# Optimization experiments

Measured on AMD Instinct MI355X. Metric: run time of the kernel, lower is better.

Reference implementation:

```python
import jax, jax.numpy as jnp
import numpy as np

N = 100000
E = 1600000
IN_F, HID_F, OUT_F = 64, 64, 32
NEG_SLOPE = 0.01  # torch F.leaky_relu default


def setup_inputs() -> dict:
    key = jax.random.key(0)
    ks = jax.random.split(key, 8)
    feats = jax.random.normal(ks[0], (N, IN_F), dtype=jnp.float32)
    edge_src = jax.random.randint(ks[1], (E,), 0, N, dtype=jnp.int32)
    edge_dst = jax.random.randint(ks[2], (E,), 0, N, dtype=jnp.int32)
    edge_weight = jax.random.uniform(ks[3], (E,), dtype=jnp.float32)
    # Linear params (torch nn.Linear init scale ~ 1/sqrt(fan_in))
    W1 = jax.random.normal(ks[4], (IN_F, HID_F), dtype=jnp.float32) / np.sqrt(IN_F)
    b1 = jnp.zeros((HID_F,), dtype=jnp.float32)
    W2 = jax.random.normal(ks[5], (HID_F, OUT_F), dtype=jnp.float32) / np.sqrt(HID_F)
    b2 = jnp.zeros((OUT_F,), dtype=jnp.float32)
    return {
        "feats": feats,
        "edge_src": edge_src,
        "edge_dst": edge_dst,
        "edge_weight": edge_weight,
        "W1": W1,
        "b1": b1,
        "W2": W2,
        "b2": b2,
    }


def _aggregate(x, edge_src, edge_dst, edge_weight):
    # (A @ x) with A given as a weighted edge list: out[dst] += w * x[src]
    msgs = x[edge_src] * edge_weight[:, None]          # [E, F]
    return jax.ops.segment_sum(msgs, edge_dst, num_segments=N)  # [N, F]


def reference(feats, edge_src, edge_dst, edge_weight, W1, b1, W2, b2):
    h = _aggregate(feats, edge_src, edge_dst, edge_weight) @ W1 + b1  # conv1(A @ feats)
    h = jnp.where(h >= 0, h, NEG_SLOPE * h)                            # leaky_relu
    h = _aggregate(h, edge_src, edge_dst, edge_weight) @ W2 + b2       # conv2(A @ h)
    return h
```

## Files before the change

### kernel.cpp

```cpp
#include <hip/hip_runtime.h>
#include <hip/hip_fp16.h>

#define NN 100000
#define NE 1600000
#define NEG_SLOPE 0.01f

#define NTL(x) __builtin_nontemporal_load(&(x))
typedef float fvec4 __attribute__((ext_vector_type(4)));
typedef float fvec2 __attribute__((ext_vector_type(2)));
typedef short bf16x8 __attribute__((ext_vector_type(8)));
typedef float f32x4 __attribute__((ext_vector_type(4)));

#define NB     391
#define TILE   4096
#define NTILES 391
#define CAP    8192

#define G1_BLOCKS 512
#define G1_WAVES  (G1_BLOCKS * 4)
#define G1_TILES  6250

#define OFF_BCNT  400384
#define OFF_BOFFS 402432
#define OFF_GCUR  404432
#define OFF_CSR   408384
#define OFF_YQ    6808384
#define OFF_HW    19608384

__global__ __launch_bounds__(256) void k_bucketcnt(const int* __restrict__ dst,
                                                   int* __restrict__ bcnt)
{
    __shared__ int h[NB];
    int t = threadIdx.x;
    for (int i = t; i < NB; i += 256) h[i] = 0;
    __syncthreads();
    int base = blockIdx.x * TILE;
    for (int i = t; i < TILE; i += 256) {
        int e = base + i;
        if (e < NE) atomicAdd(&h[NTL(dst[e]) >> 8], 1);
    }
    __syncthreads();
    for (int i = t; i < NB; i += 256)
        if (h[i]) atomicAdd(&bcnt[i], h[i]);
}

__global__ __launch_bounds__(512) void k_bucketscan(const int* __restrict__ bcnt,
                                                    int* __restrict__ boffs,
                                                    int* __restrict__ gcur)
{
    __shared__ int lds[512];
    int t = threadIdx.x;
    int v = (t < NB) ? bcnt[t] : 0;
    lds[t] = v;
    __syncthreads();
    for (int off = 1; off < 512; off <<= 1) {
        int x = (t >= off) ? lds[t - off] : 0;
        __syncthreads();
        lds[t] += x;
        __syncthreads();
    }
    int excl = lds[t] - v;
    if (t < NB) { boffs[t] = excl; gcur[t] = excl; }
    if (t == NB - 1) boffs[NB] = lds[t];
}

__global__ __launch_bounds__(256) void k_binscatter(const int* __restrict__ dst,
                                                    const int* __restrict__ esrc,
                                                    const float* __restrict__ ew,
                                                    int* __restrict__ gcur,
                                                    int2* __restrict__ binned)
{
    __shared__ int   hist[NB];
    __shared__ int   cstart[NB];
    __shared__ int   ccur[NB];
    __shared__ int   gb[NB];
    __shared__ int   lds2[256];
    __shared__ int   sdst[TILE];
    __shared__ short sbuck[TILE];
    __shared__ int2  stage[TILE];

    int t = threadIdx.x;
    int base = blockIdx.x * TILE;
    int nvalid = NE - base; if (nvalid > TILE) nvalid = TILE;

    for (int i = t; i < NB; i += 256) hist[i] = 0;
    __syncthreads();
    for (int i = t; i < TILE; i += 256) {
        int e = base + i;
        int d = (e < NE) ? NTL(dst[e]) : -1;
        sdst[i] = d;
        if (d >= 0) atomicAdd(&hist[d >> 8], 1);
    }
    __syncthreads();

    int h0 = (2 * t     < NB) ? hist[2 * t]     : 0;
    int h1 = (2 * t + 1 < NB) ? hist[2 * t + 1] : 0;
    int ps = h0 + h1;
    lds2[t] = ps;
    __syncthreads();
    for (int off = 1; off < 256; off <<= 1) {
        int x = (t >= off) ? lds2[t - off] : 0;
        __syncthreads();
        lds2[t] += x;
        __syncthreads();
    }
    int excl = lds2[t] - ps;
    if (2 * t     < NB) { cstart[2 * t]     = excl;      ccur[2 * t]     = excl; }
    if (2 * t + 1 < NB) { cstart[2 * t + 1] = excl + h0; ccur[2 * t + 1] = excl + h0; }
    __syncthreads();

    for (int i = t; i < TILE; i += 256) {
        int d = sdst[i];
        if (d >= 0) {
            int e = base + i;
            int b = d >> 8;
            int pos = atomicAdd(&ccur[b], 1);
            stage[pos] = make_int2((NTL(esrc[e]) << 8) | (d & 255),
                                   __float_as_int(NTL(ew[e])));
            sbuck[pos] = (short)b;
        }
    }
    __syncthreads();

    for (int i = t; i < NB; i += 256)
        if (hist[i]) gb[i] = atomicAdd(&gcur[i], hist[i]);
    __syncthreads();
    for (int i = t; i < nvalid; i += 256) {
        int b = sbuck[i];
        binned[gb[b] + (i - cstart[b])] = stage[i];
    }
}

__global__ __launch_bounds__(256) void k_bucketsort(const int2* __restrict__ binned,
                                                    const int* __restrict__ boffs,
                                                    int* __restrict__ offs,
                                                    int* __restrict__ csrp)
{
    __shared__ int nhist[256];
    __shared__ int nstart[256];
    __shared__ int ncur[256];
    __shared__ int lds[256];
    __shared__ int stage[CAP];

    int t = threadIdx.x, b = blockIdx.x;
    int s0 = boffs[b], s1 = boffs[b + 1];
    int cnt = s1 - s0;

    nhist[t] = 0;
    __syncthreads();
    for (int i = t; i < cnt; i += 256)
        atomicAdd(&nhist[binned[s0 + i].x & 255], 1);
    __syncthreads();

    int v = nhist[t];
    lds[t] = v;
    __syncthreads();
    for (int off = 1; off < 256; off <<= 1) {
        int x = (t >= off) ? lds[t - off] : 0;
        __syncthreads();
        lds[t] += x;
        __syncthreads();
    }
    int excl = lds[t] - v;
    nstart[t] = excl;
    ncur[t] = excl;
    int node = b * 256 + t;
    if (node < NN) offs[node] = s0 + excl;
    if (b == NB - 1 && t == 0) offs[NN] = s1;
    __syncthreads();

    for (int i = t; i < cnt; i += 256) {
        int2 r = binned[s0 + i];
        int dl = r.x & 255;
        unsigned src = ((unsigned)r.x) >> 8;
        float w = __int_as_float(r.y);
        unsigned wq = (unsigned)(w * 32767.0f + 0.5f);
        int pos = atomicAdd(&ncur[dl], 1);
        stage[pos] = (int)((src << 15) | wq);
    }
    __syncthreads();
    for (int i = t; i < cnt; i += 256)
        csrp[s0 + i] = stage[i];
}

__device__ __forceinline__ short f2bf(float x)
{
    unsigned u = __float_as_uint(x);
    u += 0x7FFFu + ((u >> 16) & 1u);
    return (short)(u >> 16);
}

__global__ __launch_bounds__(256) void k_gemm1(const float* __restrict__ feats,
                                               const float* __restrict__ W1,
                                               unsigned char* __restrict__ Yq)
{
    int lane = threadIdx.x & 63;
    int wid = (blockIdx.x * 256 + threadIdx.x) >> 6;
    int rc = lane & 15;
    int kg = lane >> 4;

    bf16x8 bfr[4][2];
    #pragma unroll
    for (int nt = 0; nt < 4; ++nt)
        #pragma unroll
        for (int kc = 0; kc < 2; ++kc) {
            int k0 = kc * 32 + kg * 8;
            #pragma unroll
            for (int b = 0; b < 8; ++b)
                bfr[nt][kc][b] = f2bf(W1[(k0 + b) * 64 + nt * 16 + rc]);
        }

    for (int t = wid; t < G1_TILES; t += G1_WAVES) {
        const float* ar = feats + (t * 16 + rc) * 64;
        bf16x8 af[2];
        #pragma unroll
        for (int kc = 0; kc < 2; ++kc) {
            const float4 v0 = *(const float4*)(ar + kc * 32 + kg * 8);
            const float4 v1 = *(const float4*)(ar + kc * 32 + kg * 8 + 4);
            af[kc][0] = f2bf(v0.x); af[kc][1] = f2bf(v0.y);
            af[kc][2] = f2bf(v0.z); af[kc][3] = f2bf(v0.w);
            af[kc][4] = f2bf(v1.x); af[kc][5] = f2bf(v1.y);
            af[kc][6] = f2bf(v1.z); af[kc][7] = f2bf(v1.w);
        }
        #pragma unroll
        for (int nt = 0; nt < 4; ++nt) {
            f32x4 acc = {0.f, 0.f, 0.f, 0.f};
            acc = __builtin_amdgcn_mfma_f32_16x16x32_bf16(af[0], bfr[nt][0], acc, 0, 0, 0);
            acc = __builtin_amdgcn_mfma_f32_16x16x32_bf16(af[1], bfr[nt][1], acc, 0, 0, 0);
            #pragma unroll
            for (int r = 0; r < 4; ++r) {
                int orow = t * 16 + kg * 4 + r;
                int b8 = __builtin_amdgcn_cvt_pk_fp8_f32(acc[r], acc[r], 0, false) & 0xFF;
                Yq[orow * 64 + nt * 16 + rc] = (unsigned char)b8;
            }
        }
    }
}

#define WDEC(c) ((float)((c) & 0x7fffu) * (1.0f / 32767.0f))

__global__ __launch_bounds__(256) void k_l1(const int* __restrict__ offs,
                                            const int* __restrict__ csrp,
                                            const unsigned char* __restrict__ Yq,
                                            const float* __restrict__ b1,
                                            const float* __restrict__ W2,
                                            __half* __restrict__ hw)
{
    __shared__ __align__(16) float sh[4][4][64];
    int tid = threadIdx.x;
    int lane = tid & 63;
    int wv = tid >> 6;
    int wid = blockIdx.x * 4 + wv;
    int n0 = wid * 4;
    int half = lane >> 5, c = lane & 31;

    float w2r[32];
    #pragma unroll
    for (int kk = 0; kk < 32; ++kk)
        w2r[kk] = W2[(half * 32 + kk) * 32 + c];

    int sub = lane >> 4;
    int e4  = lane & 15;
    const float4 bq = *(const float4*)(b1 + (e4 << 2));

    int sA = offs[n0],     eA = offs[n0 + 1];
    int sB = offs[n0 + 1], eB = offs[n0 + 2];
    int sC = offs[n0 + 2], eC = offs[n0 + 3];
    int sD = offs[n0 + 3], eD = offs[n0 + 4];

    float a0=0.f,a1=0.f,a2=0.f,a3=0.f;
    float g0=0.f,g1=0.f,g2=0.f,g3=0.f;
    float q0=0.f,q1=0.f,q2=0.f,q3=0.f;
    float r0=0.f,r1=0.f,r2=0.f,r3=0.f;
    for (int bA=sA, bB=sB, bC=sC, bD=sD;
         bA < eA || bB < eB || bC < eC || bD < eD;
         bA += 64, bB += 64, bC += 64, bD += 64) {
        int mA = eA-bA; mA = mA<0?0:(mA>64?64:mA);
        int mB = eB-bB; mB = mB<0?0:(mB>64?64:mB);
        int mC = eC-bC; mC = mC<0?0:(mC>64?64:mC);
        int mD = eD-bD; mD = mD<0?0:(mD>64?64:mD);
        int edA = (lane < mA) ? NTL(csrp[bA + lane]) : 0;
        int edB = (lane < mB) ? NTL(csrp[bB + lane]) : 0;
        int edC = (lane < mC) ? NTL(csrp[bC + lane]) : 0;
        int edD = (lane < mD) ? NTL(csrp[bD + lane]) : 0;
        int it = (mA+3)>>2;
        int t2 = (mB+3)>>2; if (t2 > it) it = t2;
        t2 = (mC+3)>>2; if (t2 > it) it = t2;
        t2 = (mD+3)>>2; if (t2 > it) it = t2;
        for (int i = 0; i < it; ++i) {
            int j = (i << 2) + sub;
            unsigned cA = (unsigned)__shfl(edA, j, 64);
            unsigned cB = (unsigned)__shfl(edB, j, 64);
            unsigned cC = (unsigned)__shfl(edC, j, 64);
            unsigned cD = (unsigned)__shfl(edD, j, 64);
            unsigned wA8 = *(const unsigned*)(Yq + (cA >> 15) * 64 + (e4 << 2));
            unsigned wB8 = *(const unsigned*)(Yq + (cB >> 15) * 64 + (e4 << 2));
            unsigned wC8 = *(const unsigned*)(Yq + (cC >> 15) * 64 + (e4 << 2));
            unsigned wD8 = *(const unsigned*)(Yq + (cD >> 15) * 64 + (e4 << 2));
            float wA = WDEC(cA), wB = WDEC(cB), wC = WDEC(cC), wD = WDEC(cD);
            fvec2 lo, hi;
            lo = __builtin_amdgcn_cvt_pk_f32_fp8((int)wA8, false);
            hi = __builtin_amdgcn_cvt_pk_f32_fp8((int)wA8, true);
            a0 = fmaf(wA, lo.x, a0); a1 = fmaf(wA, lo.y, a1);
            a2 = fmaf(wA, hi.x, a2); a3 = fmaf(wA, hi.y, a3);
            lo = __builtin_amdgcn_cvt_pk_f32_fp8((int)wB8, false);
            hi = __builtin_amdgcn_cvt_pk_f32_fp8((int)wB8, true);
            g0 = fmaf(wB, lo.x, g0); g1 = fmaf(wB, lo.y, g1);
            g2 = fmaf(wB, hi.x, g2); g3 = fmaf(wB, hi.y, g3);
            lo = __builtin_amdgcn_cvt_pk_f32_fp8((int)wC8, false);
            hi = __builtin_amdgcn_cvt_pk_f32_fp8((int)wC8, true);
            q0 = fmaf(wC, lo.x, q0); q1 = fmaf(wC, lo.y, q1);
            q2 = fmaf(wC, hi.x, q2); q3 = fmaf(wC, hi.y, q3);
            lo = __builtin_amdgcn_cvt_pk_f32_fp8((int)wD8, false);
            hi = __builtin_amdgcn_cvt_pk_f32_fp8((int)wD8, true);
            r0 = fmaf(wD, lo.x, r0); r1 = fmaf(wD, lo.y, r1);
            r2 = fmaf(wD, hi.x, r2); r3 = fmaf(wD, hi.y, r3);
        }
    }
    #define REDL1(x) x += __shfl_xor(x, 16, 64); x += __shfl_xor(x, 32, 64);
    REDL1(a0) REDL1(a1) REDL1(a2) REDL1(a3)
    REDL1(g0) REDL1(g1) REDL1(g2) REDL1(g3)
    REDL1(q0) REDL1(q1) REDL1(q2) REDL1(q3)
    REDL1(r0) REDL1(r1) REDL1(r2) REDL1(r3)

    #define LRELU(x) ((x) >= 0.f ? (x) : NEG_SLOPE * (x))
    if (sub == 0) {
        *(float4*)&sh[wv][0][e4 << 2] = make_float4(
            LRELU(a0 + bq.x), LRELU(a1 + bq.y), LRELU(a2 + bq.z), LRELU(a3 + bq.w));
        *(float4*)&sh[wv][1][e4 << 2] = make_float4(
            LRELU(g0 + bq.x), LRELU(g1 + bq.y), LRELU(g2 + bq.z), LRELU(g3 + bq.w));
        *(float4*)&sh[wv][2][e4 << 2] = make_float4(
            LRELU(q0 + bq.x), LRELU(q1 + bq.y), LRELU(q2 + bq.z), LRELU(q3 + bq.w));
        *(float4*)&sh[wv][3][e4 << 2] = make_float4(
            LRELU(r0 + bq.x), LRELU(r1 + bq.y), LRELU(r2 + bq.z), LRELU(r3 + bq.w));
    }
    __builtin_amdgcn_wave_barrier();

    float pA = 0.f, pB = 0.f, pC = 0.f, pD = 0.f;
    #pragma unroll
    for (int q = 0; q < 8; ++q) {
        float4 hvA = *(const float4*)&sh[wv][0][(half << 5) + (q << 2)];
        float4 hvB = *(const float4*)&sh[wv][1][(half << 5) + (q << 2)];
        float4 hvC = *(const float4*)&sh[wv][2][(half << 5) + (q << 2)];
        float4 hvD = *(const float4*)&sh[wv][3][(half << 5) + (q << 2)];
        pA = fmaf(hvA.x, w2r[4*q+0], pA); pB = fmaf(hvB.x, w2r[4*q+0], pB);
        pC = fmaf(hvC.x, w2r[4*q+0], pC); pD = fmaf(hvD.x, w2r[4*q+0], pD);
        pA = fmaf(hvA.y, w2r[4*q+1], pA); pB = fmaf(hvB.y, w2r[4*q+1], pB);
        pC = fmaf(hvC.y, w2r[4*q+1], pC); pD = fmaf(hvD.y, w2r[4*q+1], pD);
        pA = fmaf(hvA.z, w2r[4*q+2], pA); pB = fmaf(hvB.z, w2r[4*q+2], pB);
        pC = fmaf(hvC.z, w2r[4*q+2], pC); pD = fmaf(hvD.z, w2r[4*q+2], pD);
        pA = fmaf(hvA.w, w2r[4*q+3], pA); pB = fmaf(hvB.w, w2r[4*q+3], pB);
        pC = fmaf(hvC.w, w2r[4*q+3], pC); pD = fmaf(hvD.w, w2r[4*q+3], pD);
    }
    pA += __shfl_xor(pA, 32, 64);
    pB += __shfl_xor(pB, 32, 64);
    pC += __shfl_xor(pC, 32, 64);
    pD += __shfl_xor(pD, 32, 64);
    if (lane < 32) {
        hw[(n0 + 0) * 32 + lane] = __float2half(pA);
        hw[(n0 + 1) * 32 + lane] = __float2half(pB);
        hw[(n0 + 2) * 32 + lane] = __float2half(pC);
        hw[(n0 + 3) * 32 + lane] = __float2half(pD);
    }
}

__global__ __launch_bounds__(256) void k_l2(const int* __restrict__ offs,
                                            const int* __restrict__ csrp,
                                            const __half* __restrict__ hw,
                                            const float* __restrict__ b2,
                                            float* __restrict__ out)
{
    int tid = threadIdx.x;
    int lane = tid & 63;
    int wid = blockIdx.x * 4 + (tid >> 6);
    int n0 = wid * 4;
    int sub = lane >> 3;
    int e4  = lane & 7;
    const float4 bq = *(const float4*)(b2 + (e4 << 2));

    int sA = offs[n0],     eA = offs[n0 + 1];
    int sB = offs[n0 + 1], eB = offs[n0 + 2];
    int sC = offs[n0 + 2], eC = offs[n0 + 3];
    int sD = offs[n0 + 3], eD = offs[n0 + 4];

    float a0=0.f,a1=0.f,a2=0.f,a3=0.f;
    float g0=0.f,g1=0.f,g2=0.f,g3=0.f;
    float q0=0.f,q1=0.f,q2=0.f,q3=0.f;
    float r0=0.f,r1=0.f,r2=0.f,r3=0.f;
    for (int bA=sA, bB=sB, bC=sC, bD=sD;
         bA < eA || bB < eB || bC < eC || bD < eD;
         bA += 64, bB += 64, bC += 64, bD += 64) {
        int mA = eA-bA; mA = mA<0?0:(mA>64?64:mA);
        int mB = eB-bB; mB = mB<0?0:(mB>64?64:mB);
        int mC = eC-bC; mC = mC<0?0:(mC>64?64:mC);
        int mD = eD-bD; mD = mD<0?0:(mD>64?64:mD);
        int edA = (lane < mA) ? NTL(csrp[bA + lane]) : 0;
        int edB = (lane < mB) ? NTL(csrp[bB + lane]) : 0;
        int edC = (lane < mC) ? NTL(csrp[bC + lane]) : 0;
        int edD = (lane < mD) ? NTL(csrp[bD + lane]) : 0;
        int it = (mA+7)>>3;
        int t2 = (mB+7)>>3; if (t2 > it) it = t2;
        t2 = (mC+7)>>3; if (t2 > it) it = t2;
        t2 = (mD+7)>>3; if (t2 > it) it = t2;
        for (int i = 0; i < it; ++i) {
            int j = (i << 3) + sub;
            unsigned cA = (unsigned)__shfl(edA, j, 64);
            unsigned cB = (unsigned)__shfl(edB, j, 64);
            unsigned cC = (unsigned)__shfl(edC, j, 64);
            unsigned cD = (unsigned)__shfl(edD, j, 64);
            int2 rA = *(const int2*)(hw + (cA >> 15) * 32 + (e4 << 2));
            int2 rB = *(const int2*)(hw + (cB >> 15) * 32 + (e4 << 2));
            int2 rC = *(const int2*)(hw + (cC >> 15) * 32 + (e4 << 2));
            int2 rD = *(const int2*)(hw + (cD >> 15) * 32 + (e4 << 2));
            float wA = WDEC(cA), wB = WDEC(cB), wC = WDEC(cC), wD = WDEC(cD);
            float2 f0, f1;
            f0 = __half22float2(((const __half2*)&rA)[0]);
            f1 = __half22float2(((const __half2*)&rA)[1]);
            a0 = fmaf(wA, f0.x, a0); a1 = fmaf(wA, f0.y, a1);
            a2 = fmaf(wA, f1.x, a2); a3 = fmaf(wA, f1.y, a3);
            f0 = __half22float2(((const __half2*)&rB)[0]);
            f1 = __half22float2(((const __half2*)&rB)[1]);
            g0 = fmaf(wB, f0.x, g0); g1 = fmaf(wB, f0.y, g1);
            g2 = fmaf(wB, f1.x, g2); g3 = fmaf(wB, f1.y, g3);
            f0 = __half22float2(((const __half2*)&rC)[0]);
            f1 = __half22float2(((const __half2*)&rC)[1]);
            q0 = fmaf(wC, f0.x, q0); q1 = fmaf(wC, f0.y, q1);
            q2 = fmaf(wC, f1.x, q2); q3 = fmaf(wC, f1.y, q3);
            f0 = __half22float2(((const __half2*)&rD)[0]);
            f1 = __half22float2(((const __half2*)&rD)[1]);
            r0 = fmaf(wD, f0.x, r0); r1 = fmaf(wD, f0.y, r1);
            r2 = fmaf(wD, f1.x, r2); r3 = fmaf(wD, f1.y, r3);
        }
    }
    #define REDL2(x) x += __shfl_xor(x, 8, 64); x += __shfl_xor(x, 16, 64); \
                     x += __shfl_xor(x, 32, 64);
    REDL2(a0) REDL2(a1) REDL2(a2) REDL2(a3)
    REDL2(g0) REDL2(g1) REDL2(g2) REDL2(g3)
    REDL2(q0) REDL2(q1) REDL2(q2) REDL2(q3)
    REDL2(r0) REDL2(r1) REDL2(r2) REDL2(r3)

    if (sub == 0) {
        fvec4 oA = { a0 + bq.x, a1 + bq.y, a2 + bq.z, a3 + bq.w };
        fvec4 oB = { g0 + bq.x, g1 + bq.y, g2 + bq.z, g3 + bq.w };
        fvec4 oC = { q0 + bq.x, q1 + bq.y, q2 + bq.z, q3 + bq.w };
        fvec4 oD = { r0 + bq.x, r1 + bq.y, r2 + bq.z, r3 + bq.w };
        __builtin_nontemporal_store(oA, (fvec4*)(out + (n0+0) * 32 + (e4 << 2)));
        __builtin_nontemporal_store(oB, (fvec4*)(out + (n0+1) * 32 + (e4 << 2)));
        __builtin_nontemporal_store(oC, (fvec4*)(out + (n0+2) * 32 + (e4 << 2)));
        __builtin_nontemporal_store(oD, (fvec4*)(out + (n0+3) * 32 + (e4 << 2)));
    }
}

extern "C" void kernel_launch(void* const* d_in, const int* in_sizes, int n_in,
                              void* d_out, int out_size, void* d_ws, size_t ws_size,
                              hipStream_t stream)
{
    const float* feats = (const float*)d_in[0];
    const int*   esrc  = (const int*)d_in[1];
    const int*   edst  = (const int*)d_in[2];
    const float* ew    = (const float*)d_in[3];
    const float* W1    = (const float*)d_in[4];
    const float* b1    = (const float*)d_in[5];
    const float* W2    = (const float*)d_in[6];
    const float* b2    = (const float*)d_in[7];
    float* out = (float*)d_out;

    char*          ws     = (char*)d_ws;
    int*           offs   = (int*)ws;
    int*           bcnt   = (int*)(ws + OFF_BCNT);
    int*           boffs  = (int*)(ws + OFF_BOFFS);
    int*           gcur   = (int*)(ws + OFF_GCUR);
    int*           csrp   = (int*)(ws + OFF_CSR);
    int2*          binned = (int2*)(ws + OFF_YQ);
    unsigned char* Yq     = (unsigned char*)(ws + OFF_YQ);
    __half*        hw     = (__half*)(ws + OFF_HW);

    (void)hipMemsetAsync(bcnt, 0, NB * sizeof(int), stream);

    k_bucketcnt <<<NTILES,    256, 0, stream>>>(edst, bcnt);
    k_bucketscan<<<1,         512, 0, stream>>>(bcnt, boffs, gcur);
    k_binscatter<<<NTILES,    256, 0, stream>>>(edst, esrc, ew, gcur, binned);
    k_bucketsort<<<NB,        256, 0, stream>>>(binned, boffs, offs, csrp);
    k_gemm1     <<<G1_BLOCKS, 256, 0, stream>>>(feats, W1, Yq);
    k_l1        <<<NN / 16,   256, 0, stream>>>(offs, csrp, Yq, b1, W2, hw);
    k_l2        <<<NN / 16,   256, 0, stream>>>(offs, csrp, hw, b2, out);
}
```

Before: 144.0 us.

## Merge binscatter with gemm1 and split binned records into key and byte arrays

Folds the first GEMM into the bin-scatter launch as extra blocks, so the independent work runs concurrently and one kernel launch goes away. Weight quantization and src packing move into the scatter. The intermediate record becomes a 4-byte key plus a 1-byte local dst instead of an 8-byte int2, cutting scatter-write and bucketsort read traffic. The workspace layout is rearranged so the key/dl buffers do not alias Yq, which is now written at the same time. The fused kernel carries the larger LDS footprint of the scatter path for every block, which may reduce occupancy for the GEMM blocks.

```diff
diff --git a/kernel.cpp b/kernel.cpp
--- a/kernel.cpp
+++ b/kernel.cpp
@@ -20,12 +20,14 @@
 #define G1_WAVES  (G1_BLOCKS * 4)
 #define G1_TILES  6250
 
-#define OFF_BCNT  400384
-#define OFF_BOFFS 402432
-#define OFF_GCUR  404432
-#define OFF_CSR   408384
-#define OFF_YQ    6808384
-#define OFF_HW    19608384
+#define OFF_CSR   400384
+#define OFF_KEY   6808384
+#define OFF_DL    13208384
+#define OFF_YQ    14808384
+#define OFF_BCNT  21208384
+#define OFF_BOFFS 21210432
+#define OFF_GCUR  21212480
+#define OFF_HW    OFF_KEY
 
 __global__ __launch_bounds__(256) void k_bucketcnt(const int* __restrict__ dst,
                                                    int* __restrict__ bcnt)
@@ -64,80 +66,140 @@
     if (t == NB - 1) boffs[NB] = lds[t];
 }
 
-__global__ __launch_bounds__(256) void k_binscatter(const int* __restrict__ dst,
-                                                    const int* __restrict__ esrc,
-                                                    const float* __restrict__ ew,
-                                                    int* __restrict__ gcur,
-                                                    int2* __restrict__ binned)
-{
-    __shared__ int   hist[NB];
-    __shared__ int   cstart[NB];
-    __shared__ int   ccur[NB];
-    __shared__ int   gb[NB];
-    __shared__ int   lds2[256];
-    __shared__ int   sdst[TILE];
-    __shared__ short sbuck[TILE];
-    __shared__ int2  stage[TILE];
+__device__ __forceinline__ short f2bf(float x)
+{
+    unsigned u = __float_as_uint(x);
+    u += 0x7FFFu + ((u >> 16) & 1u);
+    return (short)(u >> 16);
+}
+
+__global__ __launch_bounds__(256) void k_bins_g1(const int* __restrict__ dst,
+                                                 const int* __restrict__ esrc,
+                                                 const float* __restrict__ ew,
+                                                 int* __restrict__ gcur,
+                                                 int* __restrict__ key,
+                                                 unsigned char* __restrict__ dl,
+                                                 const float* __restrict__ feats,
+                                                 const float* __restrict__ W1,
+                                                 unsigned char* __restrict__ Yq)
+{
+    __shared__ int           hist[NB];
+    __shared__ int           cstart[NB];
+    __shared__ int           ccur[NB];
+    __shared__ int           gb[NB];
+    __shared__ int           lds2[256];
+    __shared__ int           sdst[TILE];
+    __shared__ short         sbuck[TILE];
+    __shared__ int           stage[TILE];
+    __shared__ unsigned char sdl[TILE];
 
     int t = threadIdx.x;
-    int base = blockIdx.x * TILE;
-    int nvalid = NE - base; if (nvalid > TILE) nvalid = TILE;
-
-    for (int i = t; i < NB; i += 256) hist[i] = 0;
-    __syncthreads();
-    for (int i = t; i < TILE; i += 256) {
-        int e = base + i;
-        int d = (e < NE) ? NTL(dst[e]) : -1;
-        sdst[i] = d;
-        if (d >= 0) atomicAdd(&hist[d >> 8], 1);
-    }
-    __syncthreads();
-
-    int h0 = (2 * t     < NB) ? hist[2 * t]     : 0;
-    int h1 = (2 * t + 1 < NB) ? hist[2 * t + 1] : 0;
-    int ps = h0 + h1;
-    lds2[t] = ps;
-    __syncthreads();
-    for (int off = 1; off < 256; off <<= 1) {
-        int x = (t >= off) ? lds2[t - off] : 0;
-        __syncthreads();
-        lds2[t] += x;
-        __syncthreads();
-    }
-    int excl = lds2[t] - ps;
-    if (2 * t     < NB) { cstart[2 * t]     = excl;      ccur[2 * t]     = excl; }
-    if (2 * t + 1 < NB) { cstart[2 * t + 1] = excl + h0; ccur[2 * t + 1] = excl + h0; }
-    __syncthreads();
-
-    for (int i = t; i < TILE; i += 256) {
-        int d = sdst[i];
-        if (d >= 0) {
+
+    if (blockIdx.x < NTILES) {
+        int base = blockIdx.x * TILE;
+        int nvalid = NE - base; if (nvalid > TILE) nvalid = TILE;
+
+        for (int i = t; i < NB; i += 256) hist[i] = 0;
+        __syncthreads();
+        for (int i = t; i < TILE; i += 256) {
             int e = base + i;
-            int b = d >> 8;
-            int pos = atomicAdd(&ccur[b], 1);
-            stage[pos] = make_int2((NTL(esrc[e]) << 8) | (d & 255),
-                                   __float_as_int(NTL(ew[e])));
-            sbuck[pos] = (short)b;
-        }
-    }
-    __syncthreads();
-
-    for (int i = t; i < NB; i += 256)
-        if (hist[i]) gb[i] = atomicAdd(&gcur[i], hist[i]);
-    __syncthreads();
-    for (int i = t; i < nvalid; i += 256) {
-        int b = sbuck[i];
-        binned[gb[b] + (i - cstart[b])] = stage[i];
-    }
-}
-
-__global__ __launch_bounds__(256) void k_bucketsort(const int2* __restrict__ binned,
+            int d = (e < NE) ? NTL(dst[e]) : -1;
+            sdst[i] = d;
+            if (d >= 0) atomicAdd(&hist[d >> 8], 1);
+        }
+        __syncthreads();
+
+        int h0 = (2 * t     < NB) ? hist[2 * t]     : 0;
+        int h1 = (2 * t + 1 < NB) ? hist[2 * t + 1] : 0;
+        int ps = h0 + h1;
+        lds2[t] = ps;
+        __syncthreads();
+        for (int off = 1; off < 256; off <<= 1) {
+            int x = (t >= off) ? lds2[t - off] : 0;
+            __syncthreads();
+            lds2[t] += x;
+            __syncthreads();
+        }
+        int excl = lds2[t] - ps;
+        if (2 * t     < NB) { cstart[2 * t]     = excl;      ccur[2 * t]     = excl; }
+        if (2 * t + 1 < NB) { cstart[2 * t + 1] = excl + h0; ccur[2 * t + 1] = excl + h0; }
+        __syncthreads();
+
+        for (int i = t; i < TILE; i += 256) {
+            int d = sdst[i];
+            if (d >= 0) {
+                int e = base + i;
+                int b = d >> 8;
+                int pos = atomicAdd(&ccur[b], 1);
+                unsigned wq = (unsigned)(NTL(ew[e]) * 32767.0f + 0.5f);
+                stage[pos] = (int)(((unsigned)NTL(esrc[e]) << 15) | wq);
+                sdl[pos] = (unsigned char)(d & 255);
+                sbuck[pos] = (short)b;
+            }
+        }
+        __syncthreads();
+
+        for (int i = t; i < NB; i += 256)
+            if (hist[i]) gb[i] = atomicAdd(&gcur[i], hist[i]);
+        __syncthreads();
+        for (int i = t; i < nvalid; i += 256) {
+            int b = sbuck[i];
+            int idx = gb[b] + (i - cstart[b]);
+            key[idx] = stage[i];
+            dl[idx] = sdl[i];
+        }
+    } else {
+        int lane = t & 63;
+        int wid = ((blockIdx.x - NTILES) * 256 + t) >> 6;
+        int rc = lane & 15;
+        int kg = lane >> 4;
+
+        bf16x8 bfr[4][2];
+        #pragma unroll
+        for (int nt = 0; nt < 4; ++nt)
+            #pragma unroll
+            for (int kc = 0; kc < 2; ++kc) {
+                int k0 = kc * 32 + kg * 8;
+                #pragma unroll
+                for (int b = 0; b < 8; ++b)
+                    bfr[nt][kc][b] = f2bf(W1[(k0 + b) * 64 + nt * 16 + rc]);
+            }
+
+        for (int tt = wid; tt < G1_TILES; tt += G1_WAVES) {
+            const float* ar = feats + (tt * 16 + rc) * 64;
+            bf16x8 af[2];
+            #pragma unroll
+            for (int kc = 0; kc < 2; ++kc) {
+                const float4 v0 = *(const float4*)(ar + kc * 32 + kg * 8);
+                const float4 v1 = *(const float4*)(ar + kc * 32 + kg * 8 + 4);
+                af[kc][0] = f2bf(v0.x); af[kc][1] = f2bf(v0.y);
+                af[kc][2] = f2bf(v0.z); af[kc][3] = f2bf(v0.w);
+                af[kc][4] = f2bf(v1.x); af[kc][5] = f2bf(v1.y);
+                af[kc][6] = f2bf(v1.z); af[kc][7] = f2bf(v1.w);
+            }
+            #pragma unroll
+            for (int nt = 0; nt < 4; ++nt) {
+                f32x4 acc = {0.f, 0.f, 0.f, 0.f};
+                acc = __builtin_amdgcn_mfma_f32_16x16x32_bf16(af[0], bfr[nt][0], acc, 0, 0, 0);
+                acc = __builtin_amdgcn_mfma_f32_16x16x32_bf16(af[1], bfr[nt][1], acc, 0, 0, 0);
+                #pragma unroll
+                for (int r = 0; r < 4; ++r) {
+                    int orow = tt * 16 + kg * 4 + r;
+                    int b8 = __builtin_amdgcn_cvt_pk_fp8_f32(acc[r], acc[r], 0, false) & 0xFF;
+                    Yq[orow * 64 + nt * 16 + rc] = (unsigned char)b8;
+                }
+            }
+        }
+    }
+}
+
+__global__ __launch_bounds__(256) void k_bucketsort(const int* __restrict__ key,
+                                                    const unsigned char* __restrict__ dl,
                                                     const int* __restrict__ boffs,
                                                     int* __restrict__ offs,
                                                     int* __restrict__ csrp)
 {
     __shared__ int nhist[256];
-    __shared__ int nstart[256];
     __shared__ int ncur[256];
     __shared__ int lds[256];
     __shared__ int stage[CAP];
@@ -149,7 +211,7 @@
     nhist[t] = 0;
     __syncthreads();
     for (int i = t; i < cnt; i += 256)
-        atomicAdd(&nhist[binned[s0 + i].x & 255], 1);
+        atomicAdd(&nhist[dl[s0 + i]], 1);
     __syncthreads();
 
     int v = nhist[t];
@@ -162,7 +224,6 @@
         __syncthreads();
     }
     int excl = lds[t] - v;
-    nstart[t] = excl;
     ncur[t] = excl;
     int node = b * 256 + t;
     if (node < NN) offs[node] = s0 + excl;
@@ -170,71 +231,13 @@
     __syncthreads();
 
     for (int i = t; i < cnt; i += 256) {
-        int2 r = binned[s0 + i];
-        int dl = r.x & 255;
-        unsigned src = ((unsigned)r.x) >> 8;
-        float w = __int_as_float(r.y);
-        unsigned wq = (unsigned)(w * 32767.0f + 0.5f);
-        int pos = atomicAdd(&ncur[dl], 1);
-        stage[pos] = (int)((src << 15) | wq);
+        int d = dl[s0 + i];
+        int pos = atomicAdd(&ncur[d], 1);
+        stage[pos] = key[s0 + i];
     }
     __syncthreads();
     for (int i = t; i < cnt; i += 256)
         csrp[s0 + i] = stage[i];
-}
-
-__device__ __forceinline__ short f2bf(float x)
-{
-    unsigned u = __float_as_uint(x);
-    u += 0x7FFFu + ((u >> 16) & 1u);
-    return (short)(u >> 16);
-}
-
-__global__ __launch_bounds__(256) void k_gemm1(const float* __restrict__ feats,
-                                               const float* __restrict__ W1,
-                                               unsigned char* __restrict__ Yq)
-{
-    int lane = threadIdx.x & 63;
-    int wid = (blockIdx.x * 256 + threadIdx.x) >> 6;
-    int rc = lane & 15;
-    int kg = lane >> 4;
-
-    bf16x8 bfr[4][2];
-    #pragma unroll
-    for (int nt = 0; nt < 4; ++nt)
-        #pragma unroll
-        for (int kc = 0; kc < 2; ++kc) {
-            int k0 = kc * 32 + kg * 8;
-            #pragma unroll
-            for (int b = 0; b < 8; ++b)
-                bfr[nt][kc][b] = f2bf(W1[(k0 + b) * 64 + nt * 16 + rc]);
-        }
-
-    for (int t = wid; t < G1_TILES; t += G1_WAVES) {
-        const float* ar = feats + (t * 16 + rc) * 64;
-        bf16x8 af[2];
-        #pragma unroll
-        for (int kc = 0; kc < 2; ++kc) {
-            const float4 v0 = *(const float4*)(ar + kc * 32 + kg * 8);
-            const float4 v1 = *(const float4*)(ar + kc * 32 + kg * 8 + 4);
-            af[kc][0] = f2bf(v0.x); af[kc][1] = f2bf(v0.y);
-            af[kc][2] = f2bf(v0.z); af[kc][3] = f2bf(v0.w);
-            af[kc][4] = f2bf(v1.x); af[kc][5] = f2bf(v1.y);
-            af[kc][6] = f2bf(v1.z); af[kc][7] = f2bf(v1.w);
-        }
-        #pragma unroll
-        for (int nt = 0; nt < 4; ++nt) {
-            f32x4 acc = {0.f, 0.f, 0.f, 0.f};
-            acc = __builtin_amdgcn_mfma_f32_16x16x32_bf16(af[0], bfr[nt][0], acc, 0, 0, 0);
-            acc = __builtin_amdgcn_mfma_f32_16x16x32_bf16(af[1], bfr[nt][1], acc, 0, 0, 0);
-            #pragma unroll
-            for (int r = 0; r < 4; ++r) {
-                int orow = t * 16 + kg * 4 + r;
-                int b8 = __builtin_amdgcn_cvt_pk_fp8_f32(acc[r], acc[r], 0, false) & 0xFF;
-                Yq[orow * 64 + nt * 16 + rc] = (unsigned char)b8;
-            }
-        }
-    }
 }
 
 #define WDEC(c) ((float)((c) & 0x7fffu) * (1.0f / 32767.0f))
@@ -465,23 +468,24 @@
     const float* b2    = (const float*)d_in[7];
     float* out = (float*)d_out;
 
-    char*          ws     = (char*)d_ws;
-    int*           offs   = (int*)ws;
-    int*           bcnt   = (int*)(ws + OFF_BCNT);
-    int*           boffs  = (int*)(ws + OFF_BOFFS);
-    int*           gcur   = (int*)(ws + OFF_GCUR);
-    int*           csrp   = (int*)(ws + OFF_CSR);
-    int2*          binned = (int2*)(ws + OFF_YQ);
-    unsigned char* Yq     = (unsigned char*)(ws + OFF_YQ);
-    __half*        hw     = (__half*)(ws + OFF_HW);
+    char*          ws    = (char*)d_ws;
+    int*           offs  = (int*)ws;
+    int*           csrp  = (int*)(ws + OFF_CSR);
+    int*           key   = (int*)(ws + OFF_KEY);
+    unsigned char* dl    = (unsigned char*)(ws + OFF_DL);
+    unsigned char* Yq    = (unsigned char*)(ws + OFF_YQ);
+    int*           bcnt  = (int*)(ws + OFF_BCNT);
+    int*           boffs = (int*)(ws + OFF_BOFFS);
+    int*           gcur  = (int*)(ws + OFF_GCUR);
+    __half*        hw    = (__half*)(ws + OFF_HW);
 
     (void)hipMemsetAsync(bcnt, 0, NB * sizeof(int), stream);
 
-    k_bucketcnt <<<NTILES,    256, 0, stream>>>(edst, bcnt);
-    k_bucketscan<<<1,         512, 0, stream>>>(bcnt, boffs, gcur);
-    k_binscatter<<<NTILES,    256, 0, stream>>>(edst, esrc, ew, gcur, binned);
-    k_bucketsort<<<NB,        256, 0, stream>>>(binned, boffs, offs, csrp);
-    k_gemm1     <<<G1_BLOCKS, 256, 0, stream>>>(feats, W1, Yq);
-    k_l1        <<<NN / 16,   256, 0, stream>>>(offs, csrp, Yq, b1, W2, hw);
-    k_l2        <<<NN / 16,   256, 0, stream>>>(offs, csrp, hw, b2, out);
-}
+    k_bucketcnt <<<NTILES,             256, 0, stream>>>(edst, bcnt);
+    k_bucketscan<<<1,                  512, 0, stream>>>(bcnt, boffs, gcur);
+    k_bins_g1   <<<NTILES + G1_BLOCKS, 256, 0, stream>>>(edst, esrc, ew, gcur,
+                                                         key, dl, feats, W1, Yq);
+    k_bucketsort<<<NB,                 256, 0, stream>>>(key, dl, boffs, offs, csrp);
+    k_l1        <<<NN / 16,            256, 0, stream>>>(offs, csrp, Yq, b1, W2, hw);
+    k_l2        <<<NN / 16,            256, 0, stream>>>(offs, csrp, hw, b2, out);
+}
```

After: 140.7 us. -2.2%, faster.
